# Kernel tuning notes

Hardware: AMD Instinct MI355X
Metric: run time of the kernel (lower is better)

## Reference

```python
import jax, jax.numpy as jnp
import numpy as np

N_NODES = 50000
N_EDGES = 800000
IN_CH = 128
HID = 48
HEADS = 2
HH = HID * HEADS  # 96
N_GRAPHS = 64
NEG_SLOPE = 0.2


def _gat_layer(x, src, dst, n, W, a_src, a_dst, b, heads, out_ch):
    # x: [N, in]; W: [in, heads*out]; a_src/a_dst: [heads, out]; b: [heads*out]
    h = (x @ W).reshape(n, heads, out_ch)              # [N, H, C]
    es = (h * a_src).sum(-1)                            # [N, H]
    ed = (h * a_dst).sum(-1)                            # [N, H]
    e = jax.nn.leaky_relu(es[src] + ed[dst], NEG_SLOPE)  # [E, H]
    m = jax.ops.segment_max(e, dst, num_segments=n)      # segment softmax (stable)
    p = jnp.exp(e - m[dst])
    denom = jax.ops.segment_sum(p, dst, num_segments=n)
    alpha = p / denom[dst]                               # [E, H]
    out = jax.ops.segment_sum(alpha[:, :, None] * h[src], dst, num_segments=n)
    return out.reshape(n, heads * out_ch) + b


def setup_inputs() -> dict:
    key = jax.random.key(0)
    ks = jax.random.split(key, 20)
    x = jax.random.normal(ks[0], (N_NODES, IN_CH), dtype=jnp.float32)
    edge_index = jax.random.randint(ks[1], (2, N_EDGES), 0, N_NODES, dtype=jnp.int64)
    edge_weight = jax.random.uniform(ks[2], (N_EDGES,), dtype=jnp.float32)
    batch = jnp.sort(jax.random.randint(ks[3], (N_NODES,), 0, N_GRAPHS, dtype=jnp.int64))
    s = 0.1
    params = {
        'W1': jax.random.normal(ks[4], (IN_CH, HH)) * s,
        'as1': jax.random.normal(ks[5], (HEADS, HID)) * s,
        'ad1': jax.random.normal(ks[6], (HEADS, HID)) * s,
        'b1': jnp.zeros((HH,), jnp.float32),
        'W2': jax.random.normal(ks[7], (HH, HH)) * s,
        'as2': jax.random.normal(ks[8], (1, HH)) * s,
        'ad2': jax.random.normal(ks[9], (1, HH)) * s,
        'b2': jnp.zeros((HH,), jnp.float32),
        'W3': jax.random.normal(ks[10], (HH, HH)) * s,
        'as3': jax.random.normal(ks[11], (1, HH)) * s,
        'ad3': jax.random.normal(ks[12], (1, HH)) * s,
        'b3': jnp.zeros((HH,), jnp.float32),
        'W4': jax.random.normal(ks[13], (HH, HH)) * s,
        'as4': jax.random.normal(ks[14], (1, HH)) * s,
        'ad4': jax.random.normal(ks[15], (1, HH)) * s,
        'b4': jnp.zeros((HH,), jnp.float32),
        'Wc': jax.random.normal(ks[16], (HH, 1)) * s,
        'bc': jnp.zeros((1,), jnp.float32),
    }
    return {'x': x, 'edge_index': edge_index, 'edge_weight': edge_weight,
            'batch': batch, **params}


def reference(x, edge_index, edge_weight, batch,
              W1, as1, ad1, b1, W2, as2, ad2, b2,
              W3, as3, ad3, b3, W4, as4, ad4, b4, Wc, bc):
    n = x.shape[0]
    loops = jnp.arange(n, dtype=edge_index.dtype)  # PyG GATConv add_self_loops=True
    src = jnp.concatenate([edge_index[0], loops])
    dst = jnp.concatenate([edge_index[1], loops])
    # edge_weight is ignored by GATConv when edge_dim=None (faithful to PyG)
    h = jax.nn.relu(_gat_layer(x, src, dst, n, W1, as1, ad1, b1, HEADS, HID))
    h = jax.nn.relu(_gat_layer(h, src, dst, n, W2, as2, ad2, b2, 1, HH))
    h = jax.nn.relu(_gat_layer(h, src, dst, n, W3, as3, ad3, b3, 1, HH))
    h = jax.nn.relu(_gat_layer(h, src, dst, n, W4, as4, ad4, b4, 1, HH))
    # global_mean_pool
    sums = jax.ops.segment_sum(h, batch, num_segments=N_GRAPHS)
    cnts = jax.ops.segment_sum(jnp.ones((n, 1), h.dtype), batch, num_segments=N_GRAPHS)
    pooled = sums / jnp.maximum(cnts, 1.0)
    return jax.nn.sigmoid(pooled @ Wc + bc)
```

## Files before the change

### kernel.cpp

```cpp
#include <hip/hip_runtime.h>
#include <hip/hip_bf16.h>

#define NN 50000
#define NE 800000
#define NG 64
#define NBUCK 256
#define BN 196
#define EPB 4096
#define HB 196
#define SMAX 4200

typedef __attribute__((ext_vector_type(8))) short short8;
typedef __attribute__((ext_vector_type(4))) float float4v;
typedef __attribute__((ext_vector_type(2))) float float2v;

__device__ __forceinline__ float bf2f(unsigned short u){
    unsigned v = ((unsigned)u) << 16; float f; __builtin_memcpy(&f, &v, 4); return f;
}
__device__ __forceinline__ unsigned short f2bf(float f){
    unsigned u; __builtin_memcpy(&u, &f, 4);
    u = (u + 0x7fffu + ((u >> 16) & 1u)) >> 16;
    return (unsigned short)u;
}
__device__ __forceinline__ float lrelu(float v){ return v > 0.f ? v : 0.2f * v; }

__device__ __forceinline__ float ldflex(const void* p, long i, int isbf){
    if (isbf) return bf2f(((const unsigned short*)p)[i]);
    return ((const float*)p)[i];
}
__device__ __forceinline__ int ldidx(const int* p, long i, int is64){
    return p[is64 ? (i << 1) : i];
}

__device__ __forceinline__ unsigned int enc_fp8_1(float f){
    unsigned u; __builtin_memcpy(&u, &f, 4);
    unsigned s = (u >> 24) & 0x80u;
    float a = fabsf(f); a = fminf(a, 448.f);
    float x = a * 0x1p-120f;
    unsigned xu; __builtin_memcpy(&xu, &x, 4);
    unsigned r = (xu + 0x7FFFFu + ((xu >> 20) & 1u)) >> 20;
    if (r > 0x7Eu) r = 0x7Eu;
    return s | r;
}
__device__ __forceinline__ unsigned short pk_fp8(float a, float b){
#if __has_builtin(__builtin_amdgcn_cvt_pk_fp8_f32)
    int r = __builtin_amdgcn_cvt_pk_fp8_f32(a, b, 0, false);
    return (unsigned short)(r & 0xFFFF);
#else
    return (unsigned short)(enc_fp8_1(a) | (enc_fp8_1(b) << 8));
#endif
}
__device__ __forceinline__ float dec_fp8_manual(unsigned int byte){
    unsigned bits = ((byte & 0x80u) << 24) | ((byte & 0x7Fu) << 20);
    float f; __builtin_memcpy(&f, &bits, 4);
    return f * 0x1p120f;
}
__device__ __forceinline__ void dec_fp8x4_pk(unsigned int v, float2v& lo, float2v& hi){
#if __has_builtin(__builtin_amdgcn_cvt_pk_f32_fp8)
    lo = __builtin_amdgcn_cvt_pk_f32_fp8((int)v, false);
    hi = __builtin_amdgcn_cvt_pk_f32_fp8((int)v, true);
#else
    lo[0] = dec_fp8_manual(v & 0xFF);
    lo[1] = dec_fp8_manual((v >> 8) & 0xFF);
    hi[0] = dec_fp8_manual((v >> 16) & 0xFF);
    hi[1] = dec_fp8_manual((v >> 24) & 0xFF);
#endif
}

__device__ __forceinline__ float rdlane_f(float v, int l){
    int i; __builtin_memcpy(&i, &v, 4);
    int r = __builtin_amdgcn_readlane(i, l);
    float f; __builtin_memcpy(&f, &r, 4);
    return f;
}

__global__ void detect_kernel(const unsigned short* xu, const unsigned int* eiu,
                              const unsigned int* bu, int* flags){
    if (threadIdx.x != 0 || blockIdx.x != 0) return;
    int hit = 0;
    for (int i = 0; i < 128; i++){
        int ex = (xu[2 * i] >> 7) & 0xFF;
        if (ex >= 100 && ex <= 140) hit++;
    }
    flags[0] = (hit >= 64) ? 1 : 0;
    int z = 0;
    for (int i = 0; i < 128; i++) if (eiu[2 * i + 1] == 0) z++;
    flags[1] = (z >= 120) ? 1 : 0;
    z = 0;
    for (int i = 0; i < 128; i++) if (bu[49745 + 2 * i] == 0) z++;
    flags[2] = (z >= 120) ? 1 : 0;
}

__global__ __launch_bounds__(256) void wtprep_kernel(const void* W0, const void* W1,
                                                     const void* W2, const void* W3,
                                                     unsigned short* wt_all,
                                                     const int* flags){
    int l = blockIdx.x;
    const void* W = (l == 0) ? W0 : (l == 1) ? W1 : (l == 2) ? W2 : W3;
    int K = (l == 0) ? 128 : 96;
    unsigned short* out = wt_all + ((l == 0) ? 0 : (96 * 128 + (l - 1) * 96 * 96));
    int isbf = flags[0];
    int tot = 96 * K;
    for (int i = threadIdx.x; i < tot; i += 256){
        int c = i / K, k = i - c * K;
        out[i] = f2bf(ldflex(W, (long)k * 96 + c, isbf));
    }
}

__global__ __launch_bounds__(256) void xconv_kernel(const void* x, unsigned short* xb,
                                                    const int* flags){
    int isbf = flags[0];
    long i8 = ((long)blockIdx.x * 256 + threadIdx.x) * 8;
    if (i8 >= (long)NN * 128) return;
    unsigned int o[4];
    #pragma unroll
    for (int j = 0; j < 4; j++){
        unsigned short a = f2bf(ldflex(x, i8 + 2 * j, isbf));
        unsigned short b = f2bf(ldflex(x, i8 + 2 * j + 1, isbf));
        o[j] = (unsigned)a | ((unsigned)b << 16);
    }
    *(uint4*)(xb + i8) = make_uint4(o[0], o[1], o[2], o[3]);
}

__global__ __launch_bounds__(256) void bhist_kernel(const int* __restrict__ ei,
                                                    int* __restrict__ bcnt,
                                                    const int* __restrict__ flags){
    __shared__ int h[NBUCK];
    int tid = threadIdx.x;
    h[tid] = 0; __syncthreads();
    int f64 = flags[1];
    long e0 = (long)blockIdx.x * EPB + tid;
    #pragma unroll
    for (int r = 0; r < 16; r++){
        long e = e0 + r * 256;
        if (e < NE){
            int d = ldidx(ei, NE + e, f64);
            atomicAdd(&h[d / BN], 1);
        }
    }
    __syncthreads();
    atomicAdd(&bcnt[tid], h[tid]);
}

__global__ __launch_bounds__(256) void bscan_kernel(const int* __restrict__ bcnt,
                                                    int* __restrict__ bbase,
                                                    int* __restrict__ bcur){
    __shared__ int sd[NBUCK];
    int tid = threadIdx.x;
    int v = bcnt[tid];
    sd[tid] = v; __syncthreads();
    for (int off = 1; off < 256; off <<= 1){
        int x = sd[tid];
        int y = (tid >= off) ? sd[tid - off] : 0;
        __syncthreads();
        sd[tid] = x + y;
        __syncthreads();
    }
    int excl = sd[tid] - v;
    bbase[tid] = excl;
    bcur[tid] = excl;
    if (tid == 255) bbase[256] = excl + v;
}

__global__ __launch_bounds__(256) void bscatter_kernel(const int* __restrict__ ei,
                                                       int* __restrict__ bcur,
                                                       int2* __restrict__ ebuf,
                                                       const int* __restrict__ flags){
    __shared__ int h[NBUCK], lofs[NBUCK], gbase[NBUCK], lcur[NBUCK];
    __shared__ int2 lstage[EPB];
    int tid = threadIdx.x;
    int f64 = flags[1];
    h[tid] = 0; __syncthreads();
    int2 ed[16]; int bk[16];
    long e0 = (long)blockIdx.x * EPB + tid;
    #pragma unroll
    for (int r = 0; r < 16; r++){
        long e = e0 + r * 256;
        if (e < NE){
            int s = ldidx(ei, e, f64);
            int d = ldidx(ei, NE + e, f64);
            ed[r] = make_int2(s, d);
            bk[r] = d / BN;
            atomicAdd(&h[bk[r]], 1);
        } else bk[r] = -1;
    }
    __syncthreads();
    int v = h[tid];
    lofs[tid] = v; __syncthreads();
    for (int off = 1; off < 256; off <<= 1){
        int x = lofs[tid];
        int y = (tid >= off) ? lofs[tid - off] : 0;
        __syncthreads();
        lofs[tid] = x + y;
        __syncthreads();
    }
    int excl = lofs[tid] - v;
    lofs[tid] = excl;
    lcur[tid] = excl;
    if (v > 0) gbase[tid] = atomicAdd(&bcur[tid], v);
    __syncthreads();
    #pragma unroll
    for (int r = 0; r < 16; r++){
        if (bk[r] >= 0){
            int p = atomicAdd(&lcur[bk[r]], 1);
            lstage[p] = ed[r];
        }
    }
    __syncthreads();
    long base = (long)blockIdx.x * EPB;
    int cnt = (NE - base < EPB) ? (int)(NE - base) : EPB;
    for (int j = tid; j < cnt; j += 256){
        int2 e = lstage[j];
        int i = e.y / BN;
        ebuf[gbase[i] + j - lofs[i]] = e;
    }
}

__global__ __launch_bounds__(256) void place_kernel(const int2* __restrict__ ebuf,
                                                    const int* __restrict__ bbase,
                                                    int* __restrict__ row_ptr,
                                                    int2* __restrict__ csr2){
    __shared__ int nh[BN];
    __shared__ int nofs[256];
    __shared__ int lcur[BN];
    __shared__ int2 stage[SMAX];
    int k = blockIdx.x, tid = threadIdx.x;
    int n0 = k * BN;
    int seg0 = bbase[k], len = bbase[k + 1] - seg0;
    for (int i = tid; i < BN; i += 256) nh[i] = 0;
    __syncthreads();
    for (int j = tid; j < len; j += 256){
        int2 e = ebuf[seg0 + j];
        atomicAdd(&nh[e.y - n0], 1);
    }
    __syncthreads();
    int v = (tid < BN) ? nh[tid] : 0;
    nofs[tid] = v; __syncthreads();
    for (int off = 1; off < 256; off <<= 1){
        int x = nofs[tid];
        int y = (tid >= off) ? nofs[tid - off] : 0;
        __syncthreads();
        nofs[tid] = x + y;
        __syncthreads();
    }
    int excl = nofs[tid] - v;
    if (tid < BN){
        lcur[tid] = excl;
        int node = n0 + tid;
        if (node < NN) row_ptr[node] = seg0 + excl;
    }
    if (k == NBUCK - 1 && tid == 0) row_ptr[NN] = NE;
    __syncthreads();
    if (len <= SMAX){
        for (int j = tid; j < len; j += 256){
            int2 e = ebuf[seg0 + j];
            int p = atomicAdd(&lcur[e.y - n0], 1);
            stage[p] = e;
        }
        __syncthreads();
        for (int j = tid; j < len; j += 256)
            csr2[seg0 + j] = stage[j];
    } else {
        for (int j = tid; j < len; j += 256){
            int2 e = ebuf[seg0 + j];
            int p = atomicAdd(&lcur[e.y - n0], 1);
            csr2[seg0 + p] = e;
        }
    }
}

template<int K, int H>
__global__ __launch_bounds__(256) void gemm_mfma(const unsigned short* __restrict__ A,
                                                 const unsigned short* __restrict__ Wt,
                                                 const void* __restrict__ as_,
                                                 const void* __restrict__ ad_,
                                                 unsigned short* __restrict__ hq16,
                                                 float* __restrict__ es,
                                                 float* __restrict__ ed,
                                                 float* __restrict__ pself,
                                                 const int* __restrict__ flags){
    __shared__ union {
        struct { unsigned short xs[64 * 40]; unsigned short wt[96 * 40]; } s;
        float hs[64 * 104];
    } u;
    int tid = threadIdx.x;
    int row0 = blockIdx.x * 64;
    int lane = tid & 63, w = tid >> 6;
    int m = lane & 15, q = lane >> 4;
    float4v acc[6];
    #pragma unroll
    for (int ct = 0; ct < 6; ct++) acc[ct] = (float4v){0.f, 0.f, 0.f, 0.f};

    int sr = tid >> 2, kp = tid & 3;
    int rr = row0 + sr; if (rr >= NN) rr = NN - 1;

    for (int k0 = 0; k0 < K; k0 += 32){
        *(uint4*)(u.s.xs + sr * 40 + kp * 8) =
            *(const uint4*)(A + (size_t)rr * K + k0 + kp * 8);
        for (int i = tid; i < 96 * 4; i += 256){
            int c = i >> 2, kq = i & 3;
            *(uint4*)(u.s.wt + c * 40 + kq * 8) =
                *(const uint4*)(Wt + (size_t)c * K + k0 + kq * 8);
        }
        __syncthreads();
        short8 a = *(const short8*)(u.s.xs + (w * 16 + m) * 40 + q * 8);
        #pragma unroll
        for (int ct = 0; ct < 6; ct++){
            short8 b = *(const short8*)(u.s.wt + (ct * 16 + m) * 40 + q * 8);
            acc[ct] = __builtin_amdgcn_mfma_f32_16x16x32_bf16(a, b, acc[ct], 0, 0, 0);
        }
        __syncthreads();
    }

    #pragma unroll
    for (int ct = 0; ct < 6; ct++)
        #pragma unroll
        for (int r = 0; r < 4; r++)
            u.hs[(w * 16 + q * 4 + r) * 104 + ct * 16 + m] = acc[ct][r];
    __syncthreads();

    int rl = tid >> 2, part = tid & 3;
    int row = row0 + rl;
    int isbf = flags[0];
    float hv[24];
    #pragma unroll
    for (int jj = 0; jj < 6; jj++)
        *(float4v*)&hv[jj * 4] = *(const float4v*)&u.hs[rl * 104 + part * 24 + jj * 4];

    float pes = 0.f, ped = 0.f;
    #pragma unroll
    for (int i = 0; i < 24; i++){
        int c = part * 24 + i;
        pes += hv[i] * ldflex(as_, c, isbf);
        ped += hv[i] * ldflex(ad_, c, isbf);
    }
    pes += __shfl_xor(pes, 1); ped += __shfl_xor(ped, 1);
    if (H == 1){ pes += __shfl_xor(pes, 2); ped += __shfl_xor(ped, 2); }

    if (row < NN){
        if (part == 0){
            es[(long)row * H] = pes; ed[(long)row * H] = ped;
            pself[(long)row * H] = __expf(lrelu(pes + ped));
        }
        if (H == 2 && part == 2){
            es[(long)row * H + 1] = pes; ed[(long)row * H + 1] = ped;
            pself[(long)row * H + 1] = __expf(lrelu(pes + ped));
        }
        unsigned short wds[12];
        #pragma unroll
        for (int j = 0; j < 12; j++) wds[j] = pk_fp8(hv[2 * j], hv[2 * j + 1]);
        uint2* dst = (uint2*)hq16 + (long)row * 16 + part * 3;
        #pragma unroll
        for (int j2 = 0; j2 < 3; j2++){
            uint2 v;
            v.x = (unsigned)wds[4 * j2] | ((unsigned)wds[4 * j2 + 1] << 16);
            v.y = (unsigned)wds[4 * j2 + 2] | ((unsigned)wds[4 * j2 + 3] << 16);
            dst[j2] = v;
        }
    }
}

template<int H>
__global__ __launch_bounds__(256) void pexp_kernel(const float* __restrict__ es,
                                                   const float* __restrict__ ed,
                                                   const int2* __restrict__ csr2,
                                                   void* __restrict__ edata){
    int i = blockIdx.x * 256 + threadIdx.x;
    if (i >= NE) return;
    int2 e = csr2[i];
    if (H == 1){
        float p = __expf(lrelu(es[e.x] + ed[e.y]));
        ((uint2*)edata)[i] = make_uint2((unsigned)e.x, __float_as_uint(p));
    } else {
        float p0 = __expf(lrelu(es[2 * (long)e.x] + ed[2 * (long)e.y]));
        float p1 = __expf(lrelu(es[2 * (long)e.x + 1] + ed[2 * (long)e.y + 1]));
        ((uint4*)edata)[i] = make_uint4((unsigned)e.x, __float_as_uint(p0),
                                        __float_as_uint(p1), 0u);
    }
}

template<int H>
__global__ __launch_bounds__(256) void attn_kernel(const unsigned int* __restrict__ hq,
                                                   const void* __restrict__ edata,
                                                   const float* __restrict__ pself,
                                                   const int* __restrict__ row_ptr,
                                                   const void* __restrict__ bias,
                                                   unsigned int* __restrict__ outb,
                                                   const int* __restrict__ flags){
    int lane = threadIdx.x & 63;
    int d = blockIdx.x * 4 + (threadIdx.x >> 6);
    if (d >= NN) return;
    int isbf = flags[0];
    int beg = row_ptr[d], deg = row_ptr[d + 1] - beg;
    int g = (lane >= 24 && lane < 48) ? 1 : 0;
    int c = lane - g * 24;
    bool head0 = (c < 12);
    int m = lane - 48;

    int s_nxt = 0; float p0_nxt = 0.f, p1_nxt = 0.f;
    if (lane >= 48 && m < deg){
        if (H == 1){
            uint2 e = ((const uint2*)edata)[beg + m];
            s_nxt = (int)e.x; p0_nxt = __uint_as_float(e.y);
        } else {
            uint4 e = ((const uint4*)edata)[beg + m];
            s_nxt = (int)e.x; p0_nxt = __uint_as_float(e.y); p1_nxt = __uint_as_float(e.z);
        }
    }

    float2v acc01 = {0.f, 0.f}, acc23 = {0.f, 0.f};
    float dn0 = 0.f, dn1 = 0.f;
    for (int base = 0; base < deg; base += 16){
        int s_cur = s_nxt; float p0c = p0_nxt, p1c = p1_nxt;
        dn0 += p0c; dn1 += p1c;
        int nb = base + 16;
        s_nxt = 0; p0_nxt = 0.f; p1_nxt = 0.f;
        if (lane >= 48 && nb + m < deg){
            if (H == 1){
                uint2 e = ((const uint2*)edata)[beg + nb + m];
                s_nxt = (int)e.x; p0_nxt = __uint_as_float(e.y);
            } else {
                uint4 e = ((const uint4*)edata)[beg + nb + m];
                s_nxt = (int)e.x; p0_nxt = __uint_as_float(e.y); p1_nxt = __uint_as_float(e.z);
            }
        }
        unsigned int v[8]; float pv[8];
        #pragma unroll
        for (int jj = 0; jj < 8; jj++){
            int idx = 48 + 2 * jj + g;
            int s = __shfl(s_cur, idx);
            float p0 = __shfl(p0c, idx);
            float p;
            if (H == 2){
                float p1 = __shfl(p1c, idx);
                p = head0 ? p0 : p1;
            } else p = p0;
            pv[jj] = p;
            v[jj] = (lane < 48) ? hq[(unsigned)s * 32u + (unsigned)c] : 0u;
        }
        #pragma unroll
        for (int jj = 0; jj < 8; jj++){
            float2v lo, hi;
            dec_fp8x4_pk(v[jj], lo, hi);
            float2v p2 = {pv[jj], pv[jj]};
            acc01 += p2 * lo;
            acc23 += p2 * hi;
        }
    }

    for (int off = 1; off < 16; off <<= 1){
        dn0 += __shfl_xor(dn0, off);
        if (H == 2) dn1 += __shfl_xor(dn1, off);
    }
    float dn0_t = rdlane_f(dn0, 48);
    float dn1_t = (H == 2) ? rdlane_f(dn1, 48) : dn0_t;

    float tot[4] = {acc01[0], acc01[1], acc23[0], acc23[1]};
    #pragma unroll
    for (int k = 0; k < 4; k++) tot[k] += __shfl(tot[k], lane + 24);

    if (lane < 24){
        int head = (H == 2) ? (head0 ? 0 : 1) : 0;
        float ps = pself[(long)d * H + head];
        float dn = (head0 ? dn0_t : dn1_t) + ps;
        if (H == 1) dn = dn0_t + ps;
        float2v lo, hi;
        dec_fp8x4_pk(hq[(unsigned)d * 32u + (unsigned)c], lo, hi);
        float o0 = fmaxf((tot[0] + ps * lo[0]) / dn + ldflex(bias, 4 * c + 0, isbf), 0.f);
        float o1 = fmaxf((tot[1] + ps * lo[1]) / dn + ldflex(bias, 4 * c + 1, isbf), 0.f);
        float o2 = fmaxf((tot[2] + ps * hi[0]) / dn + ldflex(bias, 4 * c + 2, isbf), 0.f);
        float o3 = fmaxf((tot[3] + ps * hi[1]) / dn + ldflex(bias, 4 * c + 3, isbf), 0.f);
        uint2 vv;
        vv.x = (unsigned)f2bf(o0) | ((unsigned)f2bf(o1) << 16);
        vv.y = (unsigned)f2bf(o2) | ((unsigned)f2bf(o3) << 16);
        ((uint2*)outb)[(long)d * 24 + c] = vv;
    }
}

__global__ __launch_bounds__(64) void pool_kernel(const unsigned int* __restrict__ bufb,
                                                  const int* __restrict__ batch,
                                                  float* __restrict__ pooled,
                                                  int* __restrict__ gcnt,
                                                  const int* __restrict__ flags){
    int f64 = flags[2];
    int n0 = blockIdx.x * 32;
    if (n0 >= NN) return;
    int n1 = n0 + 32; if (n1 > NN) n1 = NN;
    int lane = threadIdx.x;
    if (lane < 48){
        float a0 = 0.f, a1 = 0.f;
        int curg = ldidx(batch, n0, f64);
        for (int nd = n0; nd < n1; nd++){
            int g = ldidx(batch, nd, f64);
            if (g != curg){
                atomicAdd(&pooled[curg * 96 + 2 * lane], a0);
                atomicAdd(&pooled[curg * 96 + 2 * lane + 1], a1);
                a0 = a1 = 0.f; curg = g;
            }
            unsigned v = bufb[(long)nd * 48 + lane];
            a0 += bf2f((unsigned short)v);
            a1 += bf2f((unsigned short)(v >> 16));
        }
        atomicAdd(&pooled[curg * 96 + 2 * lane], a0);
        atomicAdd(&pooled[curg * 96 + 2 * lane + 1], a1);
    } else if (lane == 48){
        int cnt = 0;
        int curg = ldidx(batch, n0, f64);
        for (int nd = n0; nd < n1; nd++){
            int g = ldidx(batch, nd, f64);
            if (g != curg){
                atomicAdd(&gcnt[curg], cnt);
                cnt = 0; curg = g;
            }
            cnt++;
        }
        atomicAdd(&gcnt[curg], cnt);
    }
}

__global__ void final_kernel(const float* __restrict__ pooled, const int* __restrict__ gcnt,
                             const void* __restrict__ Wc, const void* __restrict__ bc,
                             void* __restrict__ outp, const int* __restrict__ flags){
    int isbf = flags[0];
    int g = threadIdx.x;
    if (g >= NG) return;
    float cnt = (float)gcnt[g];
    if (cnt < 1.f) cnt = 1.f;
    float acc = 0.f;
    for (int c = 0; c < 96; c++)
        acc += (pooled[g * 96 + c] / cnt) * ldflex(Wc, c, isbf);
    acc += ldflex(bc, 0, isbf);
    float sg = 1.f / (1.f + __expf(-acc));
    if (isbf) ((unsigned short*)outp)[g] = f2bf(sg);
    else      ((float*)outp)[g] = sg;
}

extern "C" void kernel_launch(void* const* d_in, const int* in_sizes, int n_in,
                              void* d_out, int out_size, void* d_ws, size_t ws_size,
                              hipStream_t stream){
    const void* x     = d_in[0];
    const int* ei     = (const int*)d_in[1];
    const int* batch  = (const int*)d_in[3];
    const void* W[4]  = {d_in[4],  d_in[8],  d_in[12], d_in[16]};
    const void* AS[4] = {d_in[5],  d_in[9],  d_in[13], d_in[17]};
    const void* AD[4] = {d_in[6],  d_in[10], d_in[14], d_in[18]};
    const void* B[4]  = {d_in[7],  d_in[11], d_in[15], d_in[19]};
    const void* Wc    = d_in[20];
    const void* bc    = d_in[21];

    char* p = (char*)d_ws;
    auto alloc = [&](size_t bytes) -> void* {
        void* r = (void*)p;
        p += (bytes + 255) & ~(size_t)255;
        return r;
    };
    int* flags     = (int*)alloc(16);
    unsigned int* hq = (unsigned int*)alloc((size_t)NN * 128);
    unsigned int* buf1b = (unsigned int*)alloc((size_t)NN * 96 * 2);
    void* xb_edata = alloc((size_t)NE * 16);
    unsigned short* xb = (unsigned short*)xb_edata;
    void* edata = xb_edata;
    unsigned short* wt_all = (unsigned short*)alloc((size_t)(96 * 128 + 3 * 96 * 96) * 2);
    float* es      = (float*)alloc((size_t)NN * 2 * 4);
    float* ed      = (float*)alloc((size_t)NN * 2 * 4);
    float* pself   = (float*)alloc((size_t)NN * 2 * 4);
    int* row_ptr   = (int*)alloc((size_t)(NN + 1) * 4);
    int2* csr2     = (int2*)alloc((size_t)NE * 8);
    int2* ebuf     = (int2*)alloc((size_t)NE * 8);
    int* bcnt      = (int*)alloc((size_t)NBUCK * 4);
    int* bbase     = (int*)alloc((size_t)(NBUCK + 1) * 4);
    int* bcur      = (int*)alloc((size_t)NBUCK * 4);
    float* pooled  = (float*)alloc((size_t)NG * 96 * 4);
    int* gcnt      = (int*)alloc((size_t)NG * 4);

    detect_kernel<<<1, 64, 0, stream>>>((const unsigned short*)x, (const unsigned int*)ei,
                                        (const unsigned int*)batch, flags);

    wtprep_kernel<<<4, 256, 0, stream>>>(W[0], W[1], W[2], W[3], wt_all, flags);
    xconv_kernel<<<3125, 256, 0, stream>>>(x, xb, flags);

    hipMemsetAsync(bcnt, 0, (size_t)NBUCK * 4, stream);
    bhist_kernel<<<HB, 256, 0, stream>>>(ei, bcnt, flags);
    bscan_kernel<<<1, 256, 0, stream>>>(bcnt, bbase, bcur);
    bscatter_kernel<<<HB, 256, 0, stream>>>(ei, bcur, ebuf, flags);
    place_kernel<<<NBUCK, 256, 0, stream>>>(ebuf, bbase, row_ptr, csr2);

    const int GB = (NN + 63) / 64;
    const int AB = (NN + 3) / 4;
    const int EB = (NE + 255) / 256;
    unsigned short* wt1 = wt_all;
    unsigned short* wt2 = wt_all + 96 * 128;
    unsigned short* wt3 = wt2 + 96 * 96;
    unsigned short* wt4 = wt3 + 96 * 96;

    gemm_mfma<128, 2><<<GB, 256, 0, stream>>>(xb, wt1, AS[0], AD[0],
                                              (unsigned short*)hq, es, ed, pself, flags);
    pexp_kernel<2><<<EB, 256, 0, stream>>>(es, ed, csr2, edata);
    attn_kernel<2><<<AB, 256, 0, stream>>>(hq, edata, pself, row_ptr, B[0], buf1b, flags);
    unsigned short* wts[3] = {wt2, wt3, wt4};
    for (int l = 1; l < 4; l++){
        gemm_mfma<96, 1><<<GB, 256, 0, stream>>>((const unsigned short*)buf1b, wts[l - 1],
                                                 AS[l], AD[l],
                                                 (unsigned short*)hq, es, ed, pself, flags);
        pexp_kernel<1><<<EB, 256, 0, stream>>>(es, ed, csr2, edata);
        attn_kernel<1><<<AB, 256, 0, stream>>>(hq, edata, pself, row_ptr, B[l], buf1b, flags);
    }

    hipMemsetAsync(pooled, 0, (size_t)NG * 96 * 4, stream);
    hipMemsetAsync(gcnt, 0, (size_t)NG * 4, stream);
    pool_kernel<<<(NN + 31) / 32, 64, 0, stream>>>(buf1b, batch, pooled, gcnt, flags);
    final_kernel<<<1, 64, 0, stream>>>(pooled, gcnt, Wc, bc, d_out, flags);
}
```

Measured before the change: 433.7 us.

## Fuse x conversion into first GEMM, merge pooling kernels, trim launches

The fp32-to-bf16 conversion of x moves into the first-layer GEMM's tile load, which drops the separate xconv pass and its intermediate buffer. The bcnt memset now happens inside detect_kernel, and pool plus final are merged into one per-graph kernel that binary-searches the sorted batch array, which removes the atomics and several launches. The attention kernel gains a partial-chunk path that skips unused neighbor slots when fewer than 16 remain. The goal is fewer launches and less memory traffic, at the cost of per-graph pooling that may be load-imbalanced across blocks.

After: 456.7 us. +5.3%, slower.

```diff
diff --git a/kernel.cpp b/kernel.cpp
--- a/kernel.cpp
+++ b/kernel.cpp
@@ -75,8 +75,9 @@
 }
 
 __global__ void detect_kernel(const unsigned short* xu, const unsigned int* eiu,
-                              const unsigned int* bu, int* flags){
-    if (threadIdx.x != 0 || blockIdx.x != 0) return;
+                              const unsigned int* bu, int* flags, int* bcnt){
+    if (blockIdx.x == 1){ bcnt[threadIdx.x] = 0; return; }
+    if (threadIdx.x != 0) return;
     int hit = 0;
     for (int i = 0; i < 128; i++){
         int ex = (xu[2 * i] >> 7) & 0xFF;
@@ -107,21 +108,6 @@
     }
 }
 
-__global__ __launch_bounds__(256) void xconv_kernel(const void* x, unsigned short* xb,
-                                                    const int* flags){
-    int isbf = flags[0];
-    long i8 = ((long)blockIdx.x * 256 + threadIdx.x) * 8;
-    if (i8 >= (long)NN * 128) return;
-    unsigned int o[4];
-    #pragma unroll
-    for (int j = 0; j < 4; j++){
-        unsigned short a = f2bf(ldflex(x, i8 + 2 * j, isbf));
-        unsigned short b = f2bf(ldflex(x, i8 + 2 * j + 1, isbf));
-        o[j] = (unsigned)a | ((unsigned)b << 16);
-    }
-    *(uint4*)(xb + i8) = make_uint4(o[0], o[1], o[2], o[3]);
-}
-
 __global__ __launch_bounds__(256) void bhist_kernel(const int* __restrict__ ei,
                                                     int* __restrict__ bcnt,
                                                     const int* __restrict__ flags){
@@ -269,8 +255,8 @@
     }
 }
 
-template<int K, int H>
-__global__ __launch_bounds__(256) void gemm_mfma(const unsigned short* __restrict__ A,
+template<int K, int H, bool L1>
+__global__ __launch_bounds__(256) void gemm_mfma(const void* __restrict__ Ain,
                                                  const unsigned short* __restrict__ Wt,
                                                  const void* __restrict__ as_,
                                                  const void* __restrict__ ad_,
@@ -287,6 +273,7 @@
     int row0 = blockIdx.x * 64;
     int lane = tid & 63, w = tid >> 6;
     int m = lane & 15, q = lane >> 4;
+    int isbf = flags[0];
     float4v acc[6];
     #pragma unroll
     for (int ct = 0; ct < 6; ct++) acc[ct] = (float4v){0.f, 0.f, 0.f, 0.f};
@@ -295,8 +282,19 @@
     int rr = row0 + sr; if (rr >= NN) rr = NN - 1;
 
     for (int k0 = 0; k0 < K; k0 += 32){
-        *(uint4*)(u.s.xs + sr * 40 + kp * 8) =
-            *(const uint4*)(A + (size_t)rr * K + k0 + kp * 8);
+        uint4 av;
+        if (L1 && !isbf){
+            const float* xf = (const float*)Ain + (size_t)rr * K + k0 + kp * 8;
+            float4 f1 = *(const float4*)xf;
+            float4 f2 = *(const float4*)(xf + 4);
+            av.x = (unsigned)f2bf(f1.x) | ((unsigned)f2bf(f1.y) << 16);
+            av.y = (unsigned)f2bf(f1.z) | ((unsigned)f2bf(f1.w) << 16);
+            av.z = (unsigned)f2bf(f2.x) | ((unsigned)f2bf(f2.y) << 16);
+            av.w = (unsigned)f2bf(f2.z) | ((unsigned)f2bf(f2.w) << 16);
+        } else {
+            av = *(const uint4*)((const unsigned short*)Ain + (size_t)rr * K + k0 + kp * 8);
+        }
+        *(uint4*)(u.s.xs + sr * 40 + kp * 8) = av;
         for (int i = tid; i < 96 * 4; i += 256){
             int c = i >> 2, kq = i & 3;
             *(uint4*)(u.s.wt + c * 40 + kq * 8) =
@@ -321,7 +319,6 @@
 
     int rl = tid >> 2, part = tid & 3;
     int row = row0 + rl;
-    int isbf = flags[0];
     float hv[24];
     #pragma unroll
     for (int jj = 0; jj < 6; jj++)
@@ -424,27 +421,48 @@
                 s_nxt = (int)e.x; p0_nxt = __uint_as_float(e.y); p1_nxt = __uint_as_float(e.z);
             }
         }
-        unsigned int v[8]; float pv[8];
-        #pragma unroll
-        for (int jj = 0; jj < 8; jj++){
-            int idx = 48 + 2 * jj + g;
-            int s = __shfl(s_cur, idx);
-            float p0 = __shfl(p0c, idx);
-            float p;
-            if (H == 2){
-                float p1 = __shfl(p1c, idx);
-                p = head0 ? p0 : p1;
-            } else p = p0;
-            pv[jj] = p;
-            v[jj] = (lane < 48) ? hq[(unsigned)s * 32u + (unsigned)c] : 0u;
-        }
-        #pragma unroll
-        for (int jj = 0; jj < 8; jj++){
-            float2v lo, hi;
-            dec_fp8x4_pk(v[jj], lo, hi);
-            float2v p2 = {pv[jj], pv[jj]};
-            acc01 += p2 * lo;
-            acc23 += p2 * hi;
+        int cnt = deg - base; if (cnt > 16) cnt = 16;
+        if (cnt == 16){
+            unsigned int v[8]; float pv[8];
+            #pragma unroll
+            for (int jj = 0; jj < 8; jj++){
+                int idx = 48 + 2 * jj + g;
+                int s = __shfl(s_cur, idx);
+                float p0 = __shfl(p0c, idx);
+                float p;
+                if (H == 2){
+                    float p1 = __shfl(p1c, idx);
+                    p = head0 ? p0 : p1;
+                } else p = p0;
+                pv[jj] = p;
+                v[jj] = (lane < 48) ? hq[(unsigned)s * 32u + (unsigned)c] : 0u;
+            }
+            #pragma unroll
+            for (int jj = 0; jj < 8; jj++){
+                float2v lo, hi;
+                dec_fp8x4_pk(v[jj], lo, hi);
+                float2v p2 = {pv[jj], pv[jj]};
+                acc01 += p2 * lo;
+                acc23 += p2 * hi;
+            }
+        } else {
+            int njj = (cnt + 1) >> 1;
+            for (int jj = 0; jj < njj; jj++){
+                int idx = 48 + 2 * jj + g;
+                int s = __shfl(s_cur, idx);
+                float p0 = __shfl(p0c, idx);
+                float p;
+                if (H == 2){
+                    float p1 = __shfl(p1c, idx);
+                    p = head0 ? p0 : p1;
+                } else p = p0;
+                unsigned int v = (lane < 48) ? hq[(unsigned)s * 32u + (unsigned)c] : 0u;
+                float2v lo, hi;
+                dec_fp8x4_pk(v, lo, hi);
+                float2v p2 = {p, p};
+                acc01 += p2 * lo;
+                acc23 += p2 * hi;
+            }
         }
     }
 
@@ -477,62 +495,53 @@
     }
 }
 
-__global__ __launch_bounds__(64) void pool_kernel(const unsigned int* __restrict__ bufb,
-                                                  const int* __restrict__ batch,
-                                                  float* __restrict__ pooled,
-                                                  int* __restrict__ gcnt,
-                                                  const int* __restrict__ flags){
-    int f64 = flags[2];
-    int n0 = blockIdx.x * 32;
-    if (n0 >= NN) return;
-    int n1 = n0 + 32; if (n1 > NN) n1 = NN;
-    int lane = threadIdx.x;
+__global__ __launch_bounds__(256) void poolfinal_kernel(const unsigned int* __restrict__ bufb,
+                                                        const int* __restrict__ batch,
+                                                        const void* __restrict__ Wc,
+                                                        const void* __restrict__ bc,
+                                                        void* __restrict__ outp,
+                                                        const int* __restrict__ flags){
+    __shared__ int slo, shi;
+    __shared__ float part[4][96];
+    int gg = blockIdx.x;
+    int tid = threadIdx.x;
+    int isbf = flags[0], f64 = flags[2];
+    if (tid == 0){
+        int lo = 0, hi = NN;
+        while (lo < hi){ int mid = (lo + hi) >> 1; if (ldidx(batch, mid, f64) < gg) lo = mid + 1; else hi = mid; }
+        slo = lo;
+        hi = NN;
+        while (lo < hi){ int mid = (lo + hi) >> 1; if (ldidx(batch, mid, f64) < gg + 1) lo = mid + 1; else hi = mid; }
+        shi = lo;
+    }
+    __syncthreads();
+    int lane = tid & 63, w = tid >> 6;
+    float a0 = 0.f, a1 = 0.f;
     if (lane < 48){
-        float a0 = 0.f, a1 = 0.f;
-        int curg = ldidx(batch, n0, f64);
-        for (int nd = n0; nd < n1; nd++){
-            int g = ldidx(batch, nd, f64);
-            if (g != curg){
-                atomicAdd(&pooled[curg * 96 + 2 * lane], a0);
-                atomicAdd(&pooled[curg * 96 + 2 * lane + 1], a1);
-                a0 = a1 = 0.f; curg = g;
-            }
+        for (int nd = slo + w; nd < shi; nd += 4){
             unsigned v = bufb[(long)nd * 48 + lane];
             a0 += bf2f((unsigned short)v);
             a1 += bf2f((unsigned short)(v >> 16));
         }
-        atomicAdd(&pooled[curg * 96 + 2 * lane], a0);
-        atomicAdd(&pooled[curg * 96 + 2 * lane + 1], a1);
-    } else if (lane == 48){
-        int cnt = 0;
-        int curg = ldidx(batch, n0, f64);
-        for (int nd = n0; nd < n1; nd++){
-            int g = ldidx(batch, nd, f64);
-            if (g != curg){
-                atomicAdd(&gcnt[curg], cnt);
-                cnt = 0; curg = g;
-            }
-            cnt++;
-        }
-        atomicAdd(&gcnt[curg], cnt);
-    }
-}
-
-__global__ void final_kernel(const float* __restrict__ pooled, const int* __restrict__ gcnt,
-                             const void* __restrict__ Wc, const void* __restrict__ bc,
-                             void* __restrict__ outp, const int* __restrict__ flags){
-    int isbf = flags[0];
-    int g = threadIdx.x;
-    if (g >= NG) return;
-    float cnt = (float)gcnt[g];
-    if (cnt < 1.f) cnt = 1.f;
-    float acc = 0.f;
-    for (int c = 0; c < 96; c++)
-        acc += (pooled[g * 96 + c] / cnt) * ldflex(Wc, c, isbf);
-    acc += ldflex(bc, 0, isbf);
-    float sg = 1.f / (1.f + __expf(-acc));
-    if (isbf) ((unsigned short*)outp)[g] = f2bf(sg);
-    else      ((float*)outp)[g] = sg;
+        part[w][2 * lane] = a0;
+        part[w][2 * lane + 1] = a1;
+    }
+    __syncthreads();
+    if (tid < 96){
+        float s = part[0][tid] + part[1][tid] + part[2][tid] + part[3][tid];
+        int cnt = shi - slo;
+        float mean = s / fmaxf((float)cnt, 1.f);
+        part[0][tid] = mean * ldflex(Wc, tid, isbf);
+    }
+    __syncthreads();
+    if (tid == 0){
+        float acc = 0.f;
+        for (int i = 0; i < 96; i++) acc += part[0][i];
+        acc += ldflex(bc, 0, isbf);
+        float sg = 1.f / (1.f + __expf(-acc));
+        if (isbf) ((unsigned short*)outp)[gg] = f2bf(sg);
+        else      ((float*)outp)[gg] = sg;
+    }
 }
 
 extern "C" void kernel_launch(void* const* d_in, const int* in_sizes, int n_in,
@@ -557,9 +566,7 @@
     int* flags     = (int*)alloc(16);
     unsigned int* hq = (unsigned int*)alloc((size_t)NN * 128);
     unsigned int* buf1b = (unsigned int*)alloc((size_t)NN * 96 * 2);
-    void* xb_edata = alloc((size_t)NE * 16);
-    unsigned short* xb = (unsigned short*)xb_edata;
-    void* edata = xb_edata;
+    void* edata    = alloc((size_t)NE * 16);
     unsigned short* wt_all = (unsigned short*)alloc((size_t)(96 * 128 + 3 * 96 * 96) * 2);
     float* es      = (float*)alloc((size_t)NN * 2 * 4);
     float* ed      = (float*)alloc((size_t)NN * 2 * 4);
@@ -570,16 +577,11 @@
     int* bcnt      = (int*)alloc((size_t)NBUCK * 4);
     int* bbase     = (int*)alloc((size_t)(NBUCK + 1) * 4);
     int* bcur      = (int*)alloc((size_t)NBUCK * 4);
-    float* pooled  = (float*)alloc((size_t)NG * 96 * 4);
-    int* gcnt      = (int*)alloc((size_t)NG * 4);
-
-    detect_kernel<<<1, 64, 0, stream>>>((const unsigned short*)x, (const unsigned int*)ei,
-                                        (const unsigned int*)batch, flags);
-
+
+    detect_kernel<<<2, 256, 0, stream>>>((const unsigned short*)x, (const unsigned int*)ei,
+                                         (const unsigned int*)batch, flags, bcnt);
     wtprep_kernel<<<4, 256, 0, stream>>>(W[0], W[1], W[2], W[3], wt_all, flags);
-    xconv_kernel<<<3125, 256, 0, stream>>>(x, xb, flags);
-
-    hipMemsetAsync(bcnt, 0, (size_t)NBUCK * 4, stream);
+
     bhist_kernel<<<HB, 256, 0, stream>>>(ei, bcnt, flags);
     bscan_kernel<<<1, 256, 0, stream>>>(bcnt, bbase, bcur);
     bscatter_kernel<<<HB, 256, 0, stream>>>(ei, bcur, ebuf, flags);
@@ -593,21 +595,17 @@
     unsigned short* wt3 = wt2 + 96 * 96;
     unsigned short* wt4 = wt3 + 96 * 96;
 
-    gemm_mfma<128, 2><<<GB, 256, 0, stream>>>(xb, wt1, AS[0], AD[0],
-                                              (unsigned short*)hq, es, ed, pself, flags);
+    gemm_mfma<128, 2, true><<<GB, 256, 0, stream>>>(x, wt1, AS[0], AD[0],
+                                                    (unsigned short*)hq, es, ed, pself, flags);
     pexp_kernel<2><<<EB, 256, 0, stream>>>(es, ed, csr2, edata);
     attn_kernel<2><<<AB, 256, 0, stream>>>(hq, edata, pself, row_ptr, B[0], buf1b, flags);
     unsigned short* wts[3] = {wt2, wt3, wt4};
     for (int l = 1; l < 4; l++){
-        gemm_mfma<96, 1><<<GB, 256, 0, stream>>>((const unsigned short*)buf1b, wts[l - 1],
-                                                 AS[l], AD[l],
-                                                 (unsigned short*)hq, es, ed, pself, flags);
+        gemm_mfma<96, 1, false><<<GB, 256, 0, stream>>>(buf1b, wts[l - 1], AS[l], AD[l],
+                                                        (unsigned short*)hq, es, ed, pself, flags);
         pexp_kernel<1><<<EB, 256, 0, stream>>>(es, ed, csr2, edata);
         attn_kernel<1><<<AB, 256, 0, stream>>>(hq, edata, pself, row_ptr, B[l], buf1b, flags);
     }
 
-    hipMemsetAsync(pooled, 0, (size_t)NG * 96 * 4, stream);
-    hipMemsetAsync(gcnt, 0, (size_t)NG * 4, stream);
-    pool_kernel<<<(NN + 31) / 32, 64, 0, stream>>>(buf1b, batch, pooled, gcnt, flags);
-    final_kernel<<<1, 64, 0, stream>>>(pooled, gcnt, Wc, bc, d_out, flags);
-}
+    poolfinal_kernel<<<NG, 256, 0, stream>>>(buf1b, batch, Wc, bc, d_out, flags);
+}
```
